# Kernel optimization log

Hardware: AMD Instinct MI355X
Metric: run time of the kernel (lower is better)

Reference implementation:

```python
import jax, jax.numpy as jnp
import numpy as np

N_NODES = 100000
N_EDGES = 1600000
N_REL = 8
IN_CH = 128
HID = 64
OUT_CH = 128


def _rgcn_layer(x, src, dst, et, W_rel, W_root, b, num_rel):
    # x: [N, Fin]; W_rel: [R, Fin, Fout]; W_root: [Fin, Fout]; b: [Fout]
    N = x.shape[0]
    # Transform once per relation, then gather per edge (avoids per-edge matmul)
    xt = jnp.einsum('ni,rio->rno', x, W_rel)          # [R, N, Fout]
    msgs = xt[et, src]                                 # [E, Fout]
    # Per-(dst, relation) mean normalization (PyG RGCNConv aggr='mean' per relation)
    seg = dst * num_rel + et                           # combined segment id
    deg = jax.ops.segment_sum(jnp.ones_like(et, dtype=x.dtype), seg,
                              num_segments=N * num_rel)  # [N*R]
    norm = 1.0 / jnp.maximum(deg[seg], 1.0)            # [E]
    agg = jax.ops.segment_sum(msgs * norm[:, None], dst, num_segments=N)  # [N, Fout]
    return agg + x @ W_root + b


def setup_inputs() -> dict:
    key = jax.random.key(0)
    ks = jax.random.split(key, 9)
    x = jax.random.normal(ks[0], (N_NODES, IN_CH), dtype=jnp.float32)
    edge_index = jax.random.randint(ks[1], (2, N_EDGES), 0, N_NODES, dtype=jnp.int64)
    edge_type = jax.random.randint(ks[2], (N_EDGES,), 0, N_REL, dtype=jnp.int64)
    s1 = 1.0 / np.sqrt(IN_CH)
    s2 = 1.0 / np.sqrt(HID)
    W1 = jax.random.uniform(ks[3], (N_REL, IN_CH, HID), jnp.float32, -s1, s1)
    root1 = jax.random.uniform(ks[4], (IN_CH, HID), jnp.float32, -s1, s1)
    b1 = jnp.zeros((HID,), jnp.float32)
    W2 = jax.random.uniform(ks[5], (N_REL, HID, OUT_CH), jnp.float32, -s2, s2)
    root2 = jax.random.uniform(ks[6], (HID, OUT_CH), jnp.float32, -s2, s2)
    b2 = jnp.zeros((OUT_CH,), jnp.float32)
    return {"x": x, "edge_index": edge_index, "edge_type": edge_type,
            "W1": W1, "root1": root1, "b1": b1,
            "W2": W2, "root2": root2, "b2": b2}


def reference(x, edge_index, edge_type, W1, root1, b1, W2, root2, b2):
    src, dst = edge_index[0], edge_index[1]
    h = _rgcn_layer(x, src, dst, edge_type, W1, root1, b1, N_REL)
    h = jax.nn.relu(h)
    out = _rgcn_layer(h, src, dst, edge_type, W2, root2, b2, N_REL)
    return out
```

## Files before the change

### kernel.cpp

```cpp
#include <hip/hip_runtime.h>
#include <cstdint>
#include <cstddef>

#define NREL 8

typedef __attribute__((ext_vector_type(8))) short bfrag8;
typedef __attribute__((ext_vector_type(4))) float facc4;

__device__ __forceinline__ ushort f2bf(float f) {
  union { float f; uint u; } v; v.f = f;
  uint u = v.u + 0x7fffu + ((v.u >> 16) & 1u);
  return (ushort)(u >> 16);
}
__device__ __forceinline__ float bf2f(ushort u) {
  union { uint u; float f; } v; v.u = ((uint)u) << 16;
  return v.f;
}
__device__ __forceinline__ float readlane_f(float v, int l) {
  union { float f; int i; } u; u.f = v;
  u.i = __builtin_amdgcn_readlane(u.i, l);
  return u.f;
}

__global__ __launch_bounds__(256) void hist_kernel(const int* __restrict__ dst,
                                                   const int* __restrict__ et,
                                                   uint* __restrict__ hist,
                                                   uint* __restrict__ rank,
                                                   int E, int M) {
  int base = (blockIdx.x * 256 + threadIdx.x) * 8;
  if (base + 8 <= E) {
    int4 d0 = *(const int4*)&dst[base], d1 = *(const int4*)&dst[base + 4];
    int4 r0 = *(const int4*)&et[base],  r1 = *(const int4*)&et[base + 4];
    int dd[8] = {d0.x, d0.y, d0.z, d0.w, d1.x, d1.y, d1.z, d1.w};
    int rr[8] = {r0.x, r0.y, r0.z, r0.w, r1.x, r1.y, r1.z, r1.w};
    uint rk[8];
#pragma unroll
    for (int j = 0; j < 8; ++j)
      rk[j] = atomicAdd(&hist[(size_t)rr[j] * M + dd[j]], 1u);
    *(uint4*)&rank[base] = make_uint4(rk[0], rk[1], rk[2], rk[3]);
    *(uint4*)&rank[base + 4] = make_uint4(rk[4], rk[5], rk[6], rk[7]);
  } else {
    for (int j = 0; base + j < E; ++j)
      rank[base + j] = atomicAdd(&hist[(size_t)et[base + j] * M + dst[base + j]], 1u);
  }
}

__global__ __launch_bounds__(256) void scan1_kernel(const uint* __restrict__ hist,
                                                    uint* __restrict__ bsum, int M) {
  __shared__ uint r[256];
  int b = blockIdx.x, t = threadIdx.x;
  int d = b * 256 + t;
  uint s = 0;
  if (d < M) {
#pragma unroll
    for (int i = 0; i < 8; ++i) s += hist[(size_t)i * M + d];
  }
  r[t] = s; __syncthreads();
  for (int dd = 128; dd > 0; dd >>= 1) { if (t < dd) r[t] += r[t + dd]; __syncthreads(); }
  if (t == 0) bsum[b] = r[0];
}

__global__ __launch_bounds__(512) void scan2_kernel(uint* __restrict__ bsum, int nb) {
  __shared__ uint s[512];
  int t = threadIdx.x;
  uint v = (t < nb) ? bsum[t] : 0u;
  s[t] = v;
  __syncthreads();
  for (int d = 1; d < 512; d <<= 1) {
    uint add = (t >= d) ? s[t - d] : 0u;
    __syncthreads();
    s[t] += add;
    __syncthreads();
  }
  if (t < nb) bsum[t] = s[t] - v;
}

__global__ __launch_bounds__(256) void scan3_kernel(const uint* __restrict__ hist,
                                                    const uint* __restrict__ bsum,
                                                    uint* __restrict__ off,
                                                    float* __restrict__ idg,
                                                    int M, int E) {
  __shared__ uint ts[256];
  int b = blockIdx.x, t = threadIdx.x;
  int d = b * 256 + t;
  uint h[8]; uint sum = 0;
#pragma unroll
  for (int i = 0; i < 8; ++i) { h[i] = (d < M) ? hist[(size_t)i * M + d] : 0u; sum += h[i]; }
  ts[t] = sum;
  __syncthreads();
  uint own = sum;
  for (int dd = 1; dd < 256; dd <<= 1) {
    uint add = (t >= dd) ? ts[t - dd] : 0u;
    __syncthreads();
    ts[t] += add;
    __syncthreads();
  }
  uint run = bsum[b] + (ts[t] - own);
  if (d < M) {
#pragma unroll
    for (int i = 0; i < 8; ++i) {
      int k = d * 8 + i;
      off[k] = run;
      idg[k] = 1.0f / fmaxf((float)h[i], 1.0f);
      run += h[i];
    }
    if (d == M - 1) off[M * 8] = (uint)E;
  }
}

__global__ __launch_bounds__(256) void place_kernel(const int* __restrict__ src,
                                                    const int* __restrict__ dst,
                                                    const int* __restrict__ et,
                                                    const uint* __restrict__ off,
                                                    const uint* __restrict__ rank,
                                                    uint* __restrict__ sp, int E) {
  int base = (blockIdx.x * 256 + threadIdx.x) * 8;
  if (base + 8 <= E) {
    int4 d0 = *(const int4*)&dst[base], d1 = *(const int4*)&dst[base + 4];
    int4 r0 = *(const int4*)&et[base],  r1 = *(const int4*)&et[base + 4];
    int4 s0 = *(const int4*)&src[base], s1 = *(const int4*)&src[base + 4];
    uint4 k0 = *(const uint4*)&rank[base], k1 = *(const uint4*)&rank[base + 4];
    int dd[8] = {d0.x, d0.y, d0.z, d0.w, d1.x, d1.y, d1.z, d1.w};
    int rr[8] = {r0.x, r0.y, r0.z, r0.w, r1.x, r1.y, r1.z, r1.w};
    int ss[8] = {s0.x, s0.y, s0.z, s0.w, s1.x, s1.y, s1.z, s1.w};
    uint kk[8] = {k0.x, k0.y, k0.z, k0.w, k1.x, k1.y, k1.z, k1.w};
    uint oo[8];
#pragma unroll
    for (int j = 0; j < 8; ++j) oo[j] = off[(size_t)dd[j] * NREL + rr[j]];
#pragma unroll
    for (int j = 0; j < 8; ++j)
      sp[oo[j] + kk[j]] = ((uint)ss[j] << 7) | ((uint)rr[j] << 4);
  } else {
    for (int j = 0; base + j < E; ++j) {
      int e = base + j;
      int r = et[e];
      sp[off[(size_t)dst[e] * NREL + r] + rank[e]] = ((uint)src[e] << 7) | ((uint)r << 4);
    }
  }
}

__global__ __launch_bounds__(256) void cvt_wt_kernel(const float* __restrict__ in,
                                                     ushort* __restrict__ out,
                                                     int R, int K, int N) {
  int idx = blockIdx.x * 256 + threadIdx.x;
  if (idx >= R * K * N) return;
  int r = idx / (K * N);
  int rem = idx - r * K * N;
  int n = rem / K;
  int k = rem - n * K;
  out[idx] = f2bf(in[(size_t)r * K * N + (size_t)k * N + n]);
}

__global__ __launch_bounds__(256) void gemm_xt_kernel(const float* __restrict__ x,
                                                      const ushort* __restrict__ W1t,
                                                      ushort* __restrict__ xt, int M) {
  __shared__ __align__(16) ushort Axs[64][136];
  __shared__ __align__(16) ushort Bws[64][136];
  const int tid = threadIdx.x;
  const int w = tid >> 6, l = tid & 63;
  const int rows0 = blockIdx.x * 64;
#pragma unroll
  for (int i = 0; i < 8; ++i) {
    int g = tid + 256 * i;
    int row = g >> 5, c4 = (g & 31) * 4;
    int rr = rows0 + row; if (rr >= M) rr = M - 1;
    float4 v = *(const float4*)&x[(size_t)rr * 128 + c4];
    *(ushort4*)&Axs[row][c4] = make_ushort4(f2bf(v.x), f2bf(v.y), f2bf(v.z), f2bf(v.w));
  }
  __syncthreads();
  const int mrow = w * 16 + (l & 15);
  const int koff = (l >> 4) * 8;
  bfrag8 xf[4];
#pragma unroll
  for (int kc = 0; kc < 4; ++kc)
    xf[kc] = *(const bfrag8*)&Axs[mrow][kc * 32 + koff];
  const int m = rows0 + mrow;
  for (int r = 0; r < NREL; ++r) {
    __syncthreads();
#pragma unroll
    for (int i = 0; i < 8; ++i) {
      int g = tid + 256 * i;
      int row = g >> 5, c4 = (g & 31) * 4;
      *(ushort4*)&Bws[row][c4] = *(const ushort4*)&W1t[((size_t)r * 64 + row) * 128 + c4];
    }
    __syncthreads();
#pragma unroll
    for (int ct = 0; ct < 4; ++ct) {
      facc4 acc = {0.f, 0.f, 0.f, 0.f};
#pragma unroll
      for (int kc = 0; kc < 4; ++kc) {
        bfrag8 af = *(const bfrag8*)&Bws[ct * 16 + (l & 15)][kc * 32 + koff];
        acc = __builtin_amdgcn_mfma_f32_16x16x32_bf16(af, xf[kc], acc, 0, 0, 0);
      }
      if (m < M) {
        int n0 = ct * 16 + (l >> 4) * 4;
        *(ushort4*)&xt[(size_t)m * 512 + r * 64 + n0] =
            make_ushort4(f2bf(acc[0]), f2bf(acc[1]), f2bf(acc[2]), f2bf(acc[3]));
      }
    }
  }
}

__global__ __launch_bounds__(256) void agg1_kernel(const uint* __restrict__ off,
                                                   const uint* __restrict__ sp,
                                                   const float* __restrict__ idg,
                                                   const ushort* __restrict__ xt,
                                                   float* __restrict__ agg, int N) {
  int wid = (blockIdx.x * 256 + threadIdx.x) >> 6;
  if (wid >= N) return;
  int lane = threadIdx.x & 63;
  uint lane2 = (uint)lane * 2u;
  uint e0 = (uint)__builtin_amdgcn_readfirstlane((int)off[(size_t)wid * 8]);
  uint e1 = (uint)__builtin_amdgcn_readfirstlane((int)off[(size_t)wid * 8 + 8]);
  float idgl = (lane < 8) ? idg[(size_t)wid * 8 + lane] : 0.f;
  const char* xb = (const char*)xt;
  float acct = 0.f, accs = 0.f;
  uint cur = 0;
  for (uint b0 = e0; b0 < e1; b0 += 64) {
    uint vsp = sp[b0 + lane];
    uint vpr = __shfl(vsp, ((int)lane - 1) & 63);
    unsigned long long bmv = __ballot(((vsp ^ vpr) & 0x70u) != 0u);
    uint blo = (uint)__builtin_amdgcn_readfirstlane((int)(uint)bmv);
    uint bhi = (uint)__builtin_amdgcn_readfirstlane((int)(uint)(bmv >> 32));
    uint f0  = (uint)__builtin_amdgcn_readlane((int)vsp, 0);
    if ((b0 == e0) || (((f0 ^ cur) & 0x70u) != 0u)) blo |= 1u; else blo &= ~1u;
    unsigned long long sbm = (((unsigned long long)bhi) << 32) | blo;
    int n = min(64, (int)(e1 - b0));
    int i = 0;
    for (; i + 8 <= n; i += 8) {
      uint p[8]; float v[8];
#pragma unroll
      for (int j = 0; j < 8; ++j)
        p[j] = (uint)__builtin_amdgcn_readlane((int)vsp, i + j);
#pragma unroll
      for (int j = 0; j < 8; ++j)
        v[j] = bf2f(*(const ushort*)(xb + (size_t)((p[j] << 3) + lane2)));
#pragma unroll
      for (int j = 0; j < 8; ++j) {
        if ((sbm >> j) & 1ull) {
          acct += accs * readlane_f(idgl, (int)((cur >> 4) & 7u));
          accs = 0.f; cur = p[j];
        }
        accs += v[j];
      }
      sbm >>= 8;
    }
    for (; i < n; ++i) {
      uint pp = (uint)__builtin_amdgcn_readlane((int)vsp, i);
      float vv = bf2f(*(const ushort*)(xb + (size_t)((pp << 3) + lane2)));
      if (sbm & 1ull) {
        acct += accs * readlane_f(idgl, (int)((cur >> 4) & 7u));
        accs = 0.f; cur = pp;
      }
      sbm >>= 1;
      accs += vv;
    }
  }
  acct += accs * readlane_f(idgl, (int)((cur >> 4) & 7u));
  agg[(size_t)wid * 64 + lane] = acct;
}

__global__ __launch_bounds__(256) void agg2_kernel(const uint* __restrict__ off,
                                                   const uint* __restrict__ sp,
                                                   const float* __restrict__ idg,
                                                   const ushort* __restrict__ hb,
                                                   ushort* __restrict__ y2, int N) {
  int wid = (blockIdx.x * 256 + threadIdx.x) >> 6;
  if (wid >= N) return;
  int lane = threadIdx.x & 63;
  uint lane2 = (uint)lane * 2u;
  uint e0 = (uint)__builtin_amdgcn_readfirstlane((int)off[(size_t)wid * 8]);
  uint e1 = (uint)__builtin_amdgcn_readfirstlane((int)off[(size_t)wid * 8 + 8]);
  float idgl = (lane < 8) ? idg[(size_t)wid * 8 + lane] : 0.f;
  const char* hbb = (const char*)hb;
  float accs = 0.f;
  uint cur = 0;
  bool live = false;
  uint written = 0;
  for (uint b0 = e0; b0 < e1; b0 += 64) {
    uint vsp = sp[b0 + lane];
    uint vpr = __shfl(vsp, ((int)lane - 1) & 63);
    unsigned long long bmv = __ballot(((vsp ^ vpr) & 0x70u) != 0u);
    uint blo = (uint)__builtin_amdgcn_readfirstlane((int)(uint)bmv);
    uint bhi = (uint)__builtin_amdgcn_readfirstlane((int)(uint)(bmv >> 32));
    uint f0  = (uint)__builtin_amdgcn_readlane((int)vsp, 0);
    if ((b0 == e0) || (((f0 ^ cur) & 0x70u) != 0u)) blo |= 1u; else blo &= ~1u;
    unsigned long long sbm = (((unsigned long long)bhi) << 32) | blo;
    int n = min(64, (int)(e1 - b0));
    int i = 0;
    for (; i + 8 <= n; i += 8) {
      uint p[8]; float v[8];
#pragma unroll
      for (int j = 0; j < 8; ++j)
        p[j] = (uint)__builtin_amdgcn_readlane((int)vsp, i + j);
#pragma unroll
      for (int j = 0; j < 8; ++j)
        v[j] = bf2f(*(const ushort*)(hbb + (size_t)((p[j] & ~127u) + lane2)));
#pragma unroll
      for (int j = 0; j < 8; ++j) {
        if ((sbm >> j) & 1ull) {
          if (live) {
            int r = (int)((cur >> 4) & 7u);
            y2[(size_t)wid * 512 + r * 64 + lane] = f2bf(accs * readlane_f(idgl, r));
            written |= 1u << r;
          }
          accs = 0.f; cur = p[j]; live = true;
        }
        accs += v[j];
      }
      sbm >>= 8;
    }
    for (; i < n; ++i) {
      uint pp = (uint)__builtin_amdgcn_readlane((int)vsp, i);
      float vv = bf2f(*(const ushort*)(hbb + (size_t)((pp & ~127u) + lane2)));
      if (sbm & 1ull) {
        if (live) {
          int r = (int)((cur >> 4) & 7u);
          y2[(size_t)wid * 512 + r * 64 + lane] = f2bf(accs * readlane_f(idgl, r));
          written |= 1u << r;
        }
        accs = 0.f; cur = pp; live = true;
      }
      sbm >>= 1;
      accs += vv;
    }
  }
  if (live) {
    int r = (int)((cur >> 4) & 7u);
    y2[(size_t)wid * 512 + r * 64 + lane] = f2bf(accs * readlane_f(idgl, r));
    written |= 1u << r;
  }
#pragma unroll
  for (int r = 0; r < 8; ++r)
    if (!((written >> r) & 1u))
      y2[(size_t)wid * 512 + r * 64 + lane] = 0;
}

__global__ __launch_bounds__(256) void reduce_h_kernel(const float* __restrict__ x,
                                                       const ushort* __restrict__ r1t,
                                                       const float* __restrict__ b1,
                                                       const float* __restrict__ agg,
                                                       ushort* __restrict__ hb, int M) {
  __shared__ __align__(16) ushort Axs[64][136];
  __shared__ __align__(16) ushort Bws[64][136];
  const int tid = threadIdx.x;
  const int w = tid >> 6, l = tid & 63;
  const int rows0 = blockIdx.x * 64;
#pragma unroll
  for (int i = 0; i < 8; ++i) {
    int g = tid + 256 * i;
    int row = g >> 5, c4 = (g & 31) * 4;
    int rr = rows0 + row; if (rr >= M) rr = M - 1;
    float4 v = *(const float4*)&x[(size_t)rr * 128 + c4];
    *(ushort4*)&Axs[row][c4] = make_ushort4(f2bf(v.x), f2bf(v.y), f2bf(v.z), f2bf(v.w));
    *(ushort4*)&Bws[row][c4] = *(const ushort4*)&r1t[(size_t)row * 128 + c4];
  }
  __syncthreads();
  const int mrow = w * 16 + (l & 15);
  const int koff = (l >> 4) * 8;
  const int m = rows0 + mrow;
  const int mc = (m < M) ? m : (M - 1);
  bfrag8 xf[4];
#pragma unroll
  for (int kc = 0; kc < 4; ++kc)
    xf[kc] = *(const bfrag8*)&Axs[mrow][kc * 32 + koff];
  facc4 acc[4] = {};
#pragma unroll
  for (int ct = 0; ct < 4; ++ct)
#pragma unroll
    for (int kc = 0; kc < 4; ++kc) {
      bfrag8 af = *(const bfrag8*)&Bws[ct * 16 + (l & 15)][kc * 32 + koff];
      acc[ct] = __builtin_amdgcn_mfma_f32_16x16x32_bf16(af, xf[kc], acc[ct], 0, 0, 0);
    }
#pragma unroll
  for (int ct = 0; ct < 4; ++ct) {
    int n0 = ct * 16 + (l >> 4) * 4;
    float4 s4 = *(const float4*)&agg[(size_t)mc * 64 + n0];
    float4 bb = *(const float4*)&b1[n0];
    float h0 = fmaxf(acc[ct][0] + s4.x + bb.x, 0.f);
    float h1 = fmaxf(acc[ct][1] + s4.y + bb.y, 0.f);
    float h2 = fmaxf(acc[ct][2] + s4.z + bb.z, 0.f);
    float h3 = fmaxf(acc[ct][3] + s4.w + bb.w, 0.f);
    if (m < M)
      *(ushort4*)&hb[(size_t)m * 64 + n0] =
          make_ushort4(f2bf(h0), f2bf(h1), f2bf(h2), f2bf(h3));
  }
}

__global__ __launch_bounds__(256) void gemm_out_kernel(const ushort* __restrict__ hb,
                                                       const ushort* __restrict__ y2,
                                                       const ushort* __restrict__ W2t,
                                                       const ushort* __restrict__ r2t,
                                                       const float* __restrict__ b2,
                                                       float* __restrict__ out, int M) {
  __shared__ __align__(16) ushort Bws[128][72];
  const int tid = threadIdx.x;
  const int w = tid >> 6, l = tid & 63;
  const int rows0 = blockIdx.x * 64;
  const int mrow = w * 16 + (l & 15);
  const int koff = (l >> 4) * 8;
  const int m = rows0 + mrow;
  const int mc = (m < M) ? m : (M - 1);
  facc4 oacc[8] = {};
#pragma unroll
  for (int i = 0; i < 8; ++i) {
    int g = tid + 256 * i;
    int row = g >> 4, c4 = (g & 15) * 4;
    *(ushort4*)&Bws[row][c4] = *(const ushort4*)&r2t[(size_t)row * 64 + c4];
  }
  __syncthreads();
  {
    bfrag8 h0 = *(const bfrag8*)&hb[(size_t)mc * 64 + koff];
    bfrag8 h1 = *(const bfrag8*)&hb[(size_t)mc * 64 + 32 + koff];
#pragma unroll
    for (int ct = 0; ct < 8; ++ct) {
      bfrag8 a0 = *(const bfrag8*)&Bws[ct * 16 + (l & 15)][koff];
      bfrag8 a1 = *(const bfrag8*)&Bws[ct * 16 + (l & 15)][32 + koff];
      oacc[ct] = __builtin_amdgcn_mfma_f32_16x16x32_bf16(a0, h0, oacc[ct], 0, 0, 0);
      oacc[ct] = __builtin_amdgcn_mfma_f32_16x16x32_bf16(a1, h1, oacc[ct], 0, 0, 0);
    }
  }
  for (int r = 0; r < NREL; ++r) {
    __syncthreads();
#pragma unroll
    for (int i = 0; i < 8; ++i) {
      int g = tid + 256 * i;
      int row = g >> 4, c4 = (g & 15) * 4;
      *(ushort4*)&Bws[row][c4] = *(const ushort4*)&W2t[((size_t)r * 128 + row) * 64 + c4];
    }
    __syncthreads();
    bfrag8 y0 = *(const bfrag8*)&y2[(size_t)mc * 512 + r * 64 + koff];
    bfrag8 y1f = *(const bfrag8*)&y2[(size_t)mc * 512 + r * 64 + 32 + koff];
#pragma unroll
    for (int ct = 0; ct < 8; ++ct) {
      bfrag8 a0 = *(const bfrag8*)&Bws[ct * 16 + (l & 15)][koff];
      bfrag8 a1 = *(const bfrag8*)&Bws[ct * 16 + (l & 15)][32 + koff];
      oacc[ct] = __builtin_amdgcn_mfma_f32_16x16x32_bf16(a0, y0, oacc[ct], 0, 0, 0);
      oacc[ct] = __builtin_amdgcn_mfma_f32_16x16x32_bf16(a1, y1f, oacc[ct], 0, 0, 0);
    }
  }
  if (m < M) {
#pragma unroll
    for (int ct = 0; ct < 8; ++ct) {
      int n0 = ct * 16 + (l >> 4) * 4;
      float4 bb = *(const float4*)&b2[n0];
      float4 o = make_float4(oacc[ct][0] + bb.x, oacc[ct][1] + bb.y,
                             oacc[ct][2] + bb.z, oacc[ct][3] + bb.w);
      *(float4*)&out[(size_t)m * 128 + n0] = o;
    }
  }
}

extern "C" void kernel_launch(void* const* d_in, const int* in_sizes, int n_in,
                              void* d_out, int out_size, void* d_ws, size_t ws_size,
                              hipStream_t stream) {
  const float* x     = (const float*)d_in[0];
  const int*   ei    = (const int*)d_in[1];
  const int*   et    = (const int*)d_in[2];
  const float* W1    = (const float*)d_in[3];
  const float* root1 = (const float*)d_in[4];
  const float* b1    = (const float*)d_in[5];
  const float* W2    = (const float*)d_in[6];
  const float* root2 = (const float*)d_in[7];
  const float* b2    = (const float*)d_in[8];
  float* out = (float*)d_out;

  const int M = in_sizes[0] / 128;
  const int E = in_sizes[2];
  const int NS = M * NREL;
  const int* srcp = ei;
  const int* dstp = ei + E;

  auto align = [](char*& p, size_t n) { char* q = p; p += (n + 255) & ~(size_t)255; return q; };
  char* p = (char*)d_ws;
  ushort* xt   = (ushort*)align(p, (size_t)M * 512 * 2);
  float*  agg  = (float*) align(p, (size_t)M * 64 * 4);
  ushort* hb   = (ushort*)align(p, (size_t)M * 64 * 2);
  uint*   hist = (uint*)  align(p, (size_t)NS * 4);
  uint*   rank = (uint*)  align(p, (size_t)E * 4);
  uint*   off  = (uint*)  align(p, (size_t)(NS + 1) * 4);
  float*  idg  = (float*) align(p, (size_t)NS * 4);
  uint*   sp   = (uint*)  align(p, (size_t)(E + 64) * 4);
  uint*   bsum = (uint*)  align(p, 4096);
  ushort* W1t  = (ushort*)align(p, (size_t)NREL * 64 * 128 * 2);
  ushort* r1t  = (ushort*)align(p, (size_t)64 * 128 * 2);
  ushort* W2t  = (ushort*)align(p, (size_t)NREL * 128 * 64 * 2);
  ushort* r2t  = (ushort*)align(p, (size_t)128 * 64 * 2);
  ushort* y2 = xt;

  cvt_wt_kernel<<<(NREL * 128 * 64 + 255) / 256, 256, 0, stream>>>(W1, W1t, NREL, 128, 64);
  cvt_wt_kernel<<<(128 * 64 + 255) / 256, 256, 0, stream>>>(root1, r1t, 1, 128, 64);
  cvt_wt_kernel<<<(NREL * 64 * 128 + 255) / 256, 256, 0, stream>>>(W2, W2t, NREL, 64, 128);
  cvt_wt_kernel<<<(64 * 128 + 255) / 256, 256, 0, stream>>>(root2, r2t, 1, 64, 128);

  hipMemsetAsync(hist, 0, (size_t)NS * 4, stream);
  const int E8B = (int)(((long long)E + 8LL * 256 - 1) / (8LL * 256));
  hist_kernel<<<E8B, 256, 0, stream>>>(dstp, et, hist, rank, E, M);
  const int NB = (M + 255) / 256;
  scan1_kernel<<<NB, 256, 0, stream>>>(hist, bsum, M);
  scan2_kernel<<<1, 512, 0, stream>>>(bsum, NB);
  scan3_kernel<<<NB, 256, 0, stream>>>(hist, bsum, off, idg, M, E);
  place_kernel<<<E8B, 256, 0, stream>>>(srcp, dstp, et, off, rank, sp, E);

  const int MB64 = (M + 63) / 64;
  const int AGB = (M * 64 + 255) / 256;

  gemm_xt_kernel<<<MB64, 256, 0, stream>>>(x, W1t, xt, M);
  agg1_kernel<<<AGB, 256, 0, stream>>>(off, sp, idg, xt, agg, M);
  reduce_h_kernel<<<MB64, 256, 0, stream>>>(x, r1t, b1, agg, hb, M);

  agg2_kernel<<<AGB, 256, 0, stream>>>(off, sp, idg, hb, y2, M);
  gemm_out_kernel<<<MB64, 256, 0, stream>>>(hb, y2, W2t, r2t, b2, out, M);
}
```

Before: 353.4 us.

## Fuse histogram and first-layer GEMM into one launch; merge weight conversions

```diff
diff --git a/kernel.cpp b/kernel.cpp
--- a/kernel.cpp
+++ b/kernel.cpp
@@ -22,26 +22,100 @@
   return u.f;
 }
 
-__global__ __launch_bounds__(256) void hist_kernel(const int* __restrict__ dst,
-                                                   const int* __restrict__ et,
-                                                   uint* __restrict__ hist,
-                                                   uint* __restrict__ rank,
-                                                   int E, int M) {
-  int base = (blockIdx.x * 256 + threadIdx.x) * 8;
-  if (base + 8 <= E) {
-    int4 d0 = *(const int4*)&dst[base], d1 = *(const int4*)&dst[base + 4];
-    int4 r0 = *(const int4*)&et[base],  r1 = *(const int4*)&et[base + 4];
-    int dd[8] = {d0.x, d0.y, d0.z, d0.w, d1.x, d1.y, d1.z, d1.w};
-    int rr[8] = {r0.x, r0.y, r0.z, r0.w, r1.x, r1.y, r1.z, r1.w};
-    uint rk[8];
-#pragma unroll
-    for (int j = 0; j < 8; ++j)
-      rk[j] = atomicAdd(&hist[(size_t)rr[j] * M + dd[j]], 1u);
-    *(uint4*)&rank[base] = make_uint4(rk[0], rk[1], rk[2], rk[3]);
-    *(uint4*)&rank[base + 4] = make_uint4(rk[4], rk[5], rk[6], rk[7]);
-  } else {
-    for (int j = 0; base + j < E; ++j)
-      rank[base + j] = atomicAdd(&hist[(size_t)et[base + j] * M + dst[base + j]], 1u);
+__global__ __launch_bounds__(256) void cvt_all_kernel(const float* __restrict__ W1,
+                                                      const float* __restrict__ r1,
+                                                      const float* __restrict__ W2,
+                                                      const float* __restrict__ r2,
+                                                      ushort* __restrict__ W1t,
+                                                      ushort* __restrict__ r1t,
+                                                      ushort* __restrict__ W2t,
+                                                      ushort* __restrict__ r2t) {
+  int idx = blockIdx.x * 256 + threadIdx.x;
+  const float* in; ushort* out; int K, N, rel;
+  if (idx < 65536)        { in = W1; out = W1t; K = 128; N = 64;  rel = idx >> 13; idx &= 8191; }
+  else if (idx < 73728)   { idx -= 65536; in = r1; out = r1t; K = 128; N = 64; rel = 0; }
+  else if (idx < 139264)  { idx -= 73728; in = W2; out = W2t; K = 64; N = 128; rel = idx >> 13; idx &= 8191; }
+  else if (idx < 147456)  { idx -= 139264; in = r2; out = r2t; K = 64; N = 128; rel = 0; }
+  else return;
+  int n = idx / K, k = idx - n * K;
+  out[(size_t)rel * K * N + (size_t)n * K + k] =
+      f2bf(in[(size_t)rel * K * N + (size_t)k * N + n]);
+}
+
+__global__ __launch_bounds__(256) void fused1_kernel(const float* __restrict__ x,
+                                                     const ushort* __restrict__ W1t,
+                                                     ushort* __restrict__ xt,
+                                                     const int* __restrict__ dst,
+                                                     const int* __restrict__ et,
+                                                     uint* __restrict__ hist,
+                                                     uint* __restrict__ rank,
+                                                     int M, int E, int HB) {
+  __shared__ __align__(16) ushort Axs[64][136];
+  __shared__ __align__(16) ushort Bws[64][136];
+  const int bid = blockIdx.x;
+  const int hq = bid / 3;
+  if ((bid % 3) == 0 && hq < HB) {
+    int base = (hq * 256 + threadIdx.x) * 8;
+    if (base + 8 <= E) {
+      int4 d0 = *(const int4*)&dst[base], d1 = *(const int4*)&dst[base + 4];
+      int4 r0 = *(const int4*)&et[base],  r1 = *(const int4*)&et[base + 4];
+      int dd[8] = {d0.x, d0.y, d0.z, d0.w, d1.x, d1.y, d1.z, d1.w};
+      int rr[8] = {r0.x, r0.y, r0.z, r0.w, r1.x, r1.y, r1.z, r1.w};
+      uint rk[8];
+#pragma unroll
+      for (int j = 0; j < 8; ++j)
+        rk[j] = atomicAdd(&hist[(size_t)rr[j] * M + dd[j]], 1u);
+      *(uint4*)&rank[base] = make_uint4(rk[0], rk[1], rk[2], rk[3]);
+      *(uint4*)&rank[base + 4] = make_uint4(rk[4], rk[5], rk[6], rk[7]);
+    } else {
+      for (int j = 0; base + j < E; ++j)
+        rank[base + j] = atomicAdd(&hist[(size_t)et[base + j] * M + dst[base + j]], 1u);
+    }
+    return;
+  }
+  const int gidx = (hq < HB) ? (bid - hq - 1) : (bid - HB);
+  const int tid = threadIdx.x;
+  const int w = tid >> 6, l = tid & 63;
+  const int rows0 = gidx * 64;
+#pragma unroll
+  for (int i = 0; i < 8; ++i) {
+    int g = tid + 256 * i;
+    int row = g >> 5, c4 = (g & 31) * 4;
+    int rr = rows0 + row; if (rr >= M) rr = M - 1;
+    float4 v = *(const float4*)&x[(size_t)rr * 128 + c4];
+    *(ushort4*)&Axs[row][c4] = make_ushort4(f2bf(v.x), f2bf(v.y), f2bf(v.z), f2bf(v.w));
+  }
+  __syncthreads();
+  const int mrow = w * 16 + (l & 15);
+  const int koff = (l >> 4) * 8;
+  bfrag8 xf[4];
+#pragma unroll
+  for (int kc = 0; kc < 4; ++kc)
+    xf[kc] = *(const bfrag8*)&Axs[mrow][kc * 32 + koff];
+  const int m = rows0 + mrow;
+  for (int r = 0; r < NREL; ++r) {
+    __syncthreads();
+#pragma unroll
+    for (int i = 0; i < 8; ++i) {
+      int g = tid + 256 * i;
+      int row = g >> 5, c4 = (g & 31) * 4;
+      *(ushort4*)&Bws[row][c4] = *(const ushort4*)&W1t[((size_t)r * 64 + row) * 128 + c4];
+    }
+    __syncthreads();
+#pragma unroll
+    for (int ct = 0; ct < 4; ++ct) {
+      facc4 acc = {0.f, 0.f, 0.f, 0.f};
+#pragma unroll
+      for (int kc = 0; kc < 4; ++kc) {
+        bfrag8 af = *(const bfrag8*)&Bws[ct * 16 + (l & 15)][kc * 32 + koff];
+        acc = __builtin_amdgcn_mfma_f32_16x16x32_bf16(af, xf[kc], acc, 0, 0, 0);
+      }
+      if (m < M) {
+        int n0 = ct * 16 + (l >> 4) * 4;
+        *(ushort4*)&xt[(size_t)m * 512 + r * 64 + n0] =
+            make_ushort4(f2bf(acc[0]), f2bf(acc[1]), f2bf(acc[2]), f2bf(acc[3]));
+      }
+    }
   }
 }
 
@@ -135,68 +209,6 @@
       int e = base + j;
       int r = et[e];
       sp[off[(size_t)dst[e] * NREL + r] + rank[e]] = ((uint)src[e] << 7) | ((uint)r << 4);
-    }
-  }
-}
-
-__global__ __launch_bounds__(256) void cvt_wt_kernel(const float* __restrict__ in,
-                                                     ushort* __restrict__ out,
-                                                     int R, int K, int N) {
-  int idx = blockIdx.x * 256 + threadIdx.x;
-  if (idx >= R * K * N) return;
-  int r = idx / (K * N);
-  int rem = idx - r * K * N;
-  int n = rem / K;
-  int k = rem - n * K;
-  out[idx] = f2bf(in[(size_t)r * K * N + (size_t)k * N + n]);
-}
-
-__global__ __launch_bounds__(256) void gemm_xt_kernel(const float* __restrict__ x,
-                                                      const ushort* __restrict__ W1t,
-                                                      ushort* __restrict__ xt, int M) {
-  __shared__ __align__(16) ushort Axs[64][136];
-  __shared__ __align__(16) ushort Bws[64][136];
-  const int tid = threadIdx.x;
-  const int w = tid >> 6, l = tid & 63;
-  const int rows0 = blockIdx.x * 64;
-#pragma unroll
-  for (int i = 0; i < 8; ++i) {
-    int g = tid + 256 * i;
-    int row = g >> 5, c4 = (g & 31) * 4;
-    int rr = rows0 + row; if (rr >= M) rr = M - 1;
-    float4 v = *(const float4*)&x[(size_t)rr * 128 + c4];
-    *(ushort4*)&Axs[row][c4] = make_ushort4(f2bf(v.x), f2bf(v.y), f2bf(v.z), f2bf(v.w));
-  }
-  __syncthreads();
-  const int mrow = w * 16 + (l & 15);
-  const int koff = (l >> 4) * 8;
-  bfrag8 xf[4];
-#pragma unroll
-  for (int kc = 0; kc < 4; ++kc)
-    xf[kc] = *(const bfrag8*)&Axs[mrow][kc * 32 + koff];
-  const int m = rows0 + mrow;
-  for (int r = 0; r < NREL; ++r) {
-    __syncthreads();
-#pragma unroll
-    for (int i = 0; i < 8; ++i) {
-      int g = tid + 256 * i;
-      int row = g >> 5, c4 = (g & 31) * 4;
-      *(ushort4*)&Bws[row][c4] = *(const ushort4*)&W1t[((size_t)r * 64 + row) * 128 + c4];
-    }
-    __syncthreads();
-#pragma unroll
-    for (int ct = 0; ct < 4; ++ct) {
-      facc4 acc = {0.f, 0.f, 0.f, 0.f};
-#pragma unroll
-      for (int kc = 0; kc < 4; ++kc) {
-        bfrag8 af = *(const bfrag8*)&Bws[ct * 16 + (l & 15)][kc * 32 + koff];
-        acc = __builtin_amdgcn_mfma_f32_16x16x32_bf16(af, xf[kc], acc, 0, 0, 0);
-      }
-      if (m < M) {
-        int n0 = ct * 16 + (l >> 4) * 4;
-        *(ushort4*)&xt[(size_t)m * 512 + r * 64 + n0] =
-            make_ushort4(f2bf(acc[0]), f2bf(acc[1]), f2bf(acc[2]), f2bf(acc[3]));
-      }
     }
   }
 }
@@ -488,24 +500,24 @@
   ushort* r2t  = (ushort*)align(p, (size_t)128 * 64 * 2);
   ushort* y2 = xt;
 
-  cvt_wt_kernel<<<(NREL * 128 * 64 + 255) / 256, 256, 0, stream>>>(W1, W1t, NREL, 128, 64);
-  cvt_wt_kernel<<<(128 * 64 + 255) / 256, 256, 0, stream>>>(root1, r1t, 1, 128, 64);
-  cvt_wt_kernel<<<(NREL * 64 * 128 + 255) / 256, 256, 0, stream>>>(W2, W2t, NREL, 64, 128);
-  cvt_wt_kernel<<<(64 * 128 + 255) / 256, 256, 0, stream>>>(root2, r2t, 1, 64, 128);
+  cvt_all_kernel<<<(147456 + 255) / 256, 256, 0, stream>>>(W1, root1, W2, root2,
+                                                           W1t, r1t, W2t, r2t);
 
   hipMemsetAsync(hist, 0, (size_t)NS * 4, stream);
-  const int E8B = (int)(((long long)E + 8LL * 256 - 1) / (8LL * 256));
-  hist_kernel<<<E8B, 256, 0, stream>>>(dstp, et, hist, rank, E, M);
+
+  const int E8B  = (int)(((long long)E + 8LL * 256 - 1) / (8LL * 256));
+  const int MB64 = (M + 63) / 64;
+  fused1_kernel<<<E8B + MB64, 256, 0, stream>>>(x, W1t, xt, dstp, et,
+                                                hist, rank, M, E, E8B);
+
   const int NB = (M + 255) / 256;
   scan1_kernel<<<NB, 256, 0, stream>>>(hist, bsum, M);
   scan2_kernel<<<1, 512, 0, stream>>>(bsum, NB);
   scan3_kernel<<<NB, 256, 0, stream>>>(hist, bsum, off, idg, M, E);
   place_kernel<<<E8B, 256, 0, stream>>>(srcp, dstp, et, off, rank, sp, E);
 
-  const int MB64 = (M + 63) / 64;
   const int AGB = (M * 64 + 255) / 256;
 
-  gemm_xt_kernel<<<MB64, 256, 0, stream>>>(x, W1t, xt, M);
   agg1_kernel<<<AGB, 256, 0, stream>>>(off, sp, idg, xt, agg, M);
   reduce_h_kernel<<<MB64, 256, 0, stream>>>(x, r1t, b1, agg, hb, M);
 
```

Measured after the change: 321.6 us. 1.1x faster.
